# Kernel optimization log

Hardware: AMD Instinct MI355X
Metric: run time of the kernel (lower is better)

Reference implementation:

```python
import jax, jax.numpy as jnp
import numpy as np

N_NODES = 50000
N_EDGES = 800000
IN_F, HID_F, OUT_F = 96, 96, 32


def setup_inputs() -> dict:
    key = jax.random.key(0)
    k1, k2, k3, k4, k5 = jax.random.split(key, 5)
    x = jax.random.normal(k1, (N_NODES, IN_F), dtype=jnp.float32)
    src = jax.random.randint(k2, (N_EDGES,), 0, N_NODES, dtype=jnp.int32)
    dst = jax.random.randint(k3, (N_EDGES,), 0, N_NODES, dtype=jnp.int32)
    W1 = jax.random.normal(k4, (IN_F, HID_F), dtype=jnp.float32) / np.sqrt(IN_F)
    b1 = jnp.zeros((HID_F,), dtype=jnp.float32)
    W2 = jax.random.normal(k5, (HID_F, OUT_F), dtype=jnp.float32) / np.sqrt(HID_F)
    b2 = jnp.zeros((OUT_F,), dtype=jnp.float32)
    return {"x": x, "src": src, "dst": dst, "W1": W1, "b1": b1, "W2": W2, "b2": b2}


def _graph_conv(src, dst, n_nodes, h, W, b):
    # DGL GraphConv, norm='both': D_out^{-1/2} A D_in^{-1/2} h W + b
    ones = jnp.ones((src.shape[0],), dtype=h.dtype)
    deg_out = jax.ops.segment_sum(ones, src, num_segments=n_nodes)  # src out-degree
    deg_in = jax.ops.segment_sum(ones, dst, num_segments=n_nodes)   # dst in-degree
    norm_src = jax.lax.rsqrt(jnp.maximum(deg_out, 1.0))
    norm_dst = jax.lax.rsqrt(jnp.maximum(deg_in, 1.0))
    h = h * norm_src[:, None]
    msg = h[src]                                                    # [E, F] gather
    agg = jax.ops.segment_sum(msg, dst, num_segments=n_nodes)       # [N, F] scatter-add
    agg = agg * norm_dst[:, None]
    return agg @ W + b


def reference(x, src, dst, W1, b1, W2, b2):
    n = x.shape[0]
    h = _graph_conv(src, dst, n, x, W1, b1)
    h = jax.nn.relu(h)
    h = _graph_conv(src, dst, n, h, W2, b2)
    return h
```

## Files before the change

### kernel.cpp

```cpp
#include <hip/hip_runtime.h>


constexpr int NN = 50000;
constexpr int NE = 800000;
constexpr int CAP = 64;
constexpr int NNP = 50048;
constexpr int HN  = 25024;
constexpr int HW  = HN / 4;
constexpr int NCH = 2;
constexpr int NSL = 64;
constexpr int PREF_NB = (NN + 255) / 256;
constexpr int CVTW_NB = 48;
constexpr int FILL_NB = NCH * NSL;
constexpr int CVTX_NB = ((NN + 1) * 12 + 255) / 256;

using bf16x8 = __attribute__((ext_vector_type(8))) short;
using u16x8  = __attribute__((ext_vector_type(8))) unsigned short;
using f32x4  = __attribute__((ext_vector_type(4))) float;

__device__ __forceinline__ ushort f2b(float f) {
    unsigned u = __float_as_uint(f);
    u += 0x7FFFu + ((u >> 16) & 1u);
    return (ushort)(u >> 16);
}
__device__ __forceinline__ float b2f(ushort h) {
    return __uint_as_float(((unsigned)h) << 16);
}

__global__ void hist_kernel(const int* __restrict__ src, const int* __restrict__ dst,
                            unsigned char* __restrict__ pS, unsigned char* __restrict__ pD,
                            int ne) {
    __shared__ int binsS[HW];
    __shared__ int binsD[HW];
    const int ch = blockIdx.x, sl = blockIdx.y;
    const int lo = ch * HN;
    for (int i = threadIdx.x; i < HW; i += 256) { binsS[i] = 0; binsD[i] = 0; }
    __syncthreads();
    const int per4 = (ne / NSL) / 4;
    const int i0 = sl * per4;
    const int4* src4 = (const int4*)src;
    const int4* dst4 = (const int4*)dst;
    for (int i = i0 + threadIdx.x; i < i0 + per4; i += 256) {
        int4 s = src4[i];
        int4 d = dst4[i];
        unsigned u;
        u = (unsigned)(s.x - lo); if (u < HN) atomicAdd(binsS + (u >> 2), 1 << ((u & 3) * 8));
        u = (unsigned)(s.y - lo); if (u < HN) atomicAdd(binsS + (u >> 2), 1 << ((u & 3) * 8));
        u = (unsigned)(s.z - lo); if (u < HN) atomicAdd(binsS + (u >> 2), 1 << ((u & 3) * 8));
        u = (unsigned)(s.w - lo); if (u < HN) atomicAdd(binsS + (u >> 2), 1 << ((u & 3) * 8));
        u = (unsigned)(d.x - lo); if (u < HN) atomicAdd(binsD + (u >> 2), 1 << ((u & 3) * 8));
        u = (unsigned)(d.y - lo); if (u < HN) atomicAdd(binsD + (u >> 2), 1 << ((u & 3) * 8));
        u = (unsigned)(d.z - lo); if (u < HN) atomicAdd(binsD + (u >> 2), 1 << ((u & 3) * 8));
        u = (unsigned)(d.w - lo); if (u < HN) atomicAdd(binsD + (u >> 2), 1 << ((u & 3) * 8));
    }
    __syncthreads();
    int* oS = (int*)(pS + (size_t)sl * NNP + lo);
    int* oD = (int*)(pD + (size_t)sl * NNP + lo);
    for (int t = threadIdx.x; t < HW; t += 256) {
        oS[t] = binsS[t];
        oD[t] = binsD[t];
    }
}

__global__ void prefix_cvtw_kernel(const unsigned char* __restrict__ pS,
                                   unsigned char* __restrict__ pD,
                                   float* __restrict__ ns, int* __restrict__ cnt,
                                   const float* __restrict__ W1, const float* __restrict__ W2,
                                   ushort* __restrict__ W1t, ushort* __restrict__ W2t, int n) {
    int b = blockIdx.x;
    if (b < PREF_NB) {
        int i = b * 256 + threadIdx.x;
        if (i >= n) return;
        int sS = 0, run = 0;
#pragma unroll
        for (int sl = 0; sl < NSL; ++sl) {
            sS += pS[(size_t)sl * NNP + i];
            int c = pD[(size_t)sl * NNP + i];
            pD[(size_t)sl * NNP + i] = (unsigned char)run;
            run += c;
        }
        ns[i] = rsqrtf(fmaxf((float)sS, 1.0f));
        cnt[i] = run;
    } else {
        int i = (b - PREF_NB) * 256 + threadIdx.x;
        if (i < 96 * 96) {
            int k = i / 96, c = i % 96;
            W1t[c * 96 + k] = f2b(W1[i]);
        } else {
            int j = i - 96 * 96;
            int k = j / 32, c = j % 32;
            W2t[c * 96 + k] = f2b(W2[j]);
        }
    }
}

__global__ void fill_cvtx_kernel(const int* __restrict__ src, const int* __restrict__ dst,
                                 const unsigned char* __restrict__ pD,
                                 ushort* __restrict__ slots,
                                 const float* __restrict__ x, const float* __restrict__ ns,
                                 ushort* __restrict__ xh, int ne, int n) {
    __shared__ int cur[HW];
    int b = blockIdx.x;
    if (b < FILL_NB) {
        const int ch = b >> 6, sl = b & 63;
        const int lo = ch * HN;
        const int* ip = (const int*)(pD + (size_t)sl * NNP + lo);
        for (int t = threadIdx.x; t < HW; t += 256) cur[t] = ip[t];
        __syncthreads();
        const int per4 = (ne / NSL) / 4;
        const int i0 = sl * per4;
        const int4* src4 = (const int4*)src;
        const int4* dst4 = (const int4*)dst;
        for (int i = i0 + threadIdx.x; i < i0 + per4; i += 256) {
            int4 d = dst4[i];
            int4 s = src4[i];
            unsigned u; int sh, old, p;
            u = (unsigned)(d.x - lo);
            if (u < HN) { sh = (u & 3) * 8; old = atomicAdd(cur + (u >> 2), 1 << sh);
                p = (old >> sh) & 0xFF; if (p < CAP) slots[((size_t)(lo + u) << 6) + p] = (ushort)s.x; }
            u = (unsigned)(d.y - lo);
            if (u < HN) { sh = (u & 3) * 8; old = atomicAdd(cur + (u >> 2), 1 << sh);
                p = (old >> sh) & 0xFF; if (p < CAP) slots[((size_t)(lo + u) << 6) + p] = (ushort)s.y; }
            u = (unsigned)(d.z - lo);
            if (u < HN) { sh = (u & 3) * 8; old = atomicAdd(cur + (u >> 2), 1 << sh);
                p = (old >> sh) & 0xFF; if (p < CAP) slots[((size_t)(lo + u) << 6) + p] = (ushort)s.z; }
            u = (unsigned)(d.w - lo);
            if (u < HN) { sh = (u & 3) * 8; old = atomicAdd(cur + (u >> 2), 1 << sh);
                p = (old >> sh) & 0xFF; if (p < CAP) slots[((size_t)(lo + u) << 6) + p] = (ushort)s.w; }
        }
    } else {
        int t = (b - FILL_NB) * 256 + threadIdx.x;
        if (t >= (n + 1) * 12) return;
        int r = t / 12;
        u16x8 o;
        if (r == n) {
#pragma unroll
            for (int u = 0; u < 8; ++u) o[u] = 0;
        } else {
            float s = ns[r];
            const float4* p = (const float4*)(x) + (size_t)t * 2;
            float4 v0 = p[0], v1 = p[1];
            o[0] = f2b(s * v0.x); o[1] = f2b(s * v0.y); o[2] = f2b(s * v0.z); o[3] = f2b(s * v0.w);
            o[4] = f2b(s * v1.x); o[5] = f2b(s * v1.y); o[6] = f2b(s * v1.z); o[7] = f2b(s * v1.w);
        }
        *(u16x8*)&xh[(size_t)t * 8] = o;
    }
}

__global__ void agg1_kernel(const ushort* __restrict__ xh, const int* __restrict__ cnt,
                            const ushort* __restrict__ slots, ushort* __restrict__ AB, int n) {
    int tid = blockIdx.x * 256 + threadIdx.x;
    int r = tid / 12, q = tid % 12;
    if (r >= n) return;
    int deg = min(cnt[r], CAP);
    const ushort* br = slots + ((size_t)r << 6);
    float acc[8] = {};
    for (int j0 = 0; j0 < deg; j0 += 8) {
        u16x8 sl8 = *(const u16x8*)(br + j0);
        int s0 = (j0 + 0 < deg) ? (int)sl8[0] : n;
        int s1 = (j0 + 1 < deg) ? (int)sl8[1] : n;
        int s2 = (j0 + 2 < deg) ? (int)sl8[2] : n;
        int s3 = (j0 + 3 < deg) ? (int)sl8[3] : n;
        int s4 = (j0 + 4 < deg) ? (int)sl8[4] : n;
        int s5 = (j0 + 5 < deg) ? (int)sl8[5] : n;
        int s6 = (j0 + 6 < deg) ? (int)sl8[6] : n;
        int s7 = (j0 + 7 < deg) ? (int)sl8[7] : n;
        u16x8 v0 = *(const u16x8*)&xh[(size_t)s0 * 96 + q * 8];
        u16x8 v1 = *(const u16x8*)&xh[(size_t)s1 * 96 + q * 8];
        u16x8 v2 = *(const u16x8*)&xh[(size_t)s2 * 96 + q * 8];
        u16x8 v3 = *(const u16x8*)&xh[(size_t)s3 * 96 + q * 8];
        u16x8 v4 = *(const u16x8*)&xh[(size_t)s4 * 96 + q * 8];
        u16x8 v5 = *(const u16x8*)&xh[(size_t)s5 * 96 + q * 8];
        u16x8 v6 = *(const u16x8*)&xh[(size_t)s6 * 96 + q * 8];
        u16x8 v7 = *(const u16x8*)&xh[(size_t)s7 * 96 + q * 8];
#pragma unroll
        for (int t = 0; t < 8; ++t) acc[t] += b2f(v0[t]);
#pragma unroll
        for (int t = 0; t < 8; ++t) acc[t] += b2f(v1[t]);
#pragma unroll
        for (int t = 0; t < 8; ++t) acc[t] += b2f(v2[t]);
#pragma unroll
        for (int t = 0; t < 8; ++t) acc[t] += b2f(v3[t]);
#pragma unroll
        for (int t = 0; t < 8; ++t) acc[t] += b2f(v4[t]);
#pragma unroll
        for (int t = 0; t < 8; ++t) acc[t] += b2f(v5[t]);
#pragma unroll
        for (int t = 0; t < 8; ++t) acc[t] += b2f(v6[t]);
#pragma unroll
        for (int t = 0; t < 8; ++t) acc[t] += b2f(v7[t]);
    }
    u16x8 o;
#pragma unroll
    for (int t = 0; t < 8; ++t) o[t] = f2b(acc[t]);
    *(u16x8*)&AB[(size_t)r * 96 + q * 8] = o;
}

__global__ void __launch_bounds__(256) gemm12_fused(
        const ushort* __restrict__ AB, const ushort* __restrict__ W1t,
        const ushort* __restrict__ W2t, const float* __restrict__ b1,
        const float* __restrict__ ns, const int* __restrict__ cnt,
        ushort* __restrict__ t2h, int n) {
    __shared__ ushort Wl1[96 * 104];
    __shared__ ushort Wl2[32 * 104];
    __shared__ ushort Hl[64 * 104];
    for (int i = threadIdx.x; i < 1152; i += 256) {
        int nr = i / 12, k = (i % 12) * 8;
        *(bf16x8*)&Wl1[nr * 104 + k] = *(const bf16x8*)&W1t[nr * 96 + k];
    }
    for (int i = threadIdx.x; i < 384; i += 256) {
        int nr = i / 12, k = (i % 12) * 8;
        *(bf16x8*)&Wl2[nr * 104 + k] = *(const bf16x8*)&W2t[nr * 96 + k];
    }
    __syncthreads();

    const int lane = threadIdx.x & 63;
    const int w = threadIdx.x >> 6;
    const int rl = lane & 15, kg = lane >> 4;
    const int rowbase = blockIdx.x * 64 + w * 16;

    const ushort* arow = AB + (size_t)(rowbase + rl) * 96 + kg * 8;
    bf16x8 a0 = *(const bf16x8*)(arow);
    bf16x8 a1 = *(const bf16x8*)(arow + 32);
    bf16x8 a2 = *(const bf16x8*)(arow + 64);
    f32x4 acc1[6] = {};
#pragma unroll
    for (int nt = 0; nt < 6; ++nt) {
        const ushort* wr = &Wl1[(nt * 16 + rl) * 104 + kg * 8];
        acc1[nt] = __builtin_amdgcn_mfma_f32_16x16x32_bf16(a0, *(const bf16x8*)(wr),      acc1[nt], 0, 0, 0);
        acc1[nt] = __builtin_amdgcn_mfma_f32_16x16x32_bf16(a1, *(const bf16x8*)(wr + 32), acc1[nt], 0, 0, 0);
        acc1[nt] = __builtin_amdgcn_mfma_f32_16x16x32_bf16(a2, *(const bf16x8*)(wr + 64), acc1[nt], 0, 0, 0);
    }
    const int r0 = rowbase + kg * 4;
    float sj[4];
#pragma unroll
    for (int j = 0; j < 4; ++j) sj[j] = rsqrtf(fmaxf((float)cnt[r0 + j], 1.0f));
#pragma unroll
    for (int nt = 0; nt < 6; ++nt) {
        int col = nt * 16 + rl;
        float bc = b1[col];
#pragma unroll
        for (int j = 0; j < 4; ++j)
            Hl[(w * 16 + kg * 4 + j) * 104 + col] = f2b(fmaxf(acc1[nt][j] * sj[j] + bc, 0.f));
    }
    __syncthreads();

    const ushort* hrow = &Hl[(w * 16 + rl) * 104 + kg * 8];
    bf16x8 h0 = *(const bf16x8*)(hrow);
    bf16x8 h1 = *(const bf16x8*)(hrow + 32);
    bf16x8 h2 = *(const bf16x8*)(hrow + 64);
    f32x4 acc2[2] = {};
#pragma unroll
    for (int nt = 0; nt < 2; ++nt) {
        const ushort* wr = &Wl2[(nt * 16 + rl) * 104 + kg * 8];
        acc2[nt] = __builtin_amdgcn_mfma_f32_16x16x32_bf16(h0, *(const bf16x8*)(wr),      acc2[nt], 0, 0, 0);
        acc2[nt] = __builtin_amdgcn_mfma_f32_16x16x32_bf16(h1, *(const bf16x8*)(wr + 32), acc2[nt], 0, 0, 0);
        acc2[nt] = __builtin_amdgcn_mfma_f32_16x16x32_bf16(h2, *(const bf16x8*)(wr + 64), acc2[nt], 0, 0, 0);
    }
    float sn[4];
#pragma unroll
    for (int j = 0; j < 4; ++j) sn[j] = ns[r0 + j];
#pragma unroll
    for (int nt = 0; nt < 2; ++nt) {
        int col = nt * 16 + rl;
#pragma unroll
        for (int j = 0; j < 4; ++j) {
            float val = (r0 + j < n) ? acc2[nt][j] * sn[j] : 0.f;
            t2h[(size_t)(r0 + j) * 32 + col] = f2b(val);
        }
    }
}

__global__ void agg2_kernel(const ushort* __restrict__ t2h, const float* __restrict__ b2,
                            const int* __restrict__ cnt, const ushort* __restrict__ slots,
                            float* __restrict__ out, int n) {
    int tid = blockIdx.x * 256 + threadIdx.x;
    int r = tid / 4, q = tid % 4;
    if (r >= n) return;
    int deg = min(cnt[r], CAP);
    const ushort* br = slots + ((size_t)r << 6);
    float acc[8] = {};
    for (int j0 = 0; j0 < deg; j0 += 8) {
        u16x8 sl8 = *(const u16x8*)(br + j0);
        int s0 = (j0 + 0 < deg) ? (int)sl8[0] : n;
        int s1 = (j0 + 1 < deg) ? (int)sl8[1] : n;
        int s2 = (j0 + 2 < deg) ? (int)sl8[2] : n;
        int s3 = (j0 + 3 < deg) ? (int)sl8[3] : n;
        int s4 = (j0 + 4 < deg) ? (int)sl8[4] : n;
        int s5 = (j0 + 5 < deg) ? (int)sl8[5] : n;
        int s6 = (j0 + 6 < deg) ? (int)sl8[6] : n;
        int s7 = (j0 + 7 < deg) ? (int)sl8[7] : n;
        u16x8 v0 = *(const u16x8*)&t2h[(size_t)s0 * 32 + q * 8];
        u16x8 v1 = *(const u16x8*)&t2h[(size_t)s1 * 32 + q * 8];
        u16x8 v2 = *(const u16x8*)&t2h[(size_t)s2 * 32 + q * 8];
        u16x8 v3 = *(const u16x8*)&t2h[(size_t)s3 * 32 + q * 8];
        u16x8 v4 = *(const u16x8*)&t2h[(size_t)s4 * 32 + q * 8];
        u16x8 v5 = *(const u16x8*)&t2h[(size_t)s5 * 32 + q * 8];
        u16x8 v6 = *(const u16x8*)&t2h[(size_t)s6 * 32 + q * 8];
        u16x8 v7 = *(const u16x8*)&t2h[(size_t)s7 * 32 + q * 8];
#pragma unroll
        for (int t = 0; t < 8; ++t) acc[t] += b2f(v0[t]);
#pragma unroll
        for (int t = 0; t < 8; ++t) acc[t] += b2f(v1[t]);
#pragma unroll
        for (int t = 0; t < 8; ++t) acc[t] += b2f(v2[t]);
#pragma unroll
        for (int t = 0; t < 8; ++t) acc[t] += b2f(v3[t]);
#pragma unroll
        for (int t = 0; t < 8; ++t) acc[t] += b2f(v4[t]);
#pragma unroll
        for (int t = 0; t < 8; ++t) acc[t] += b2f(v5[t]);
#pragma unroll
        for (int t = 0; t < 8; ++t) acc[t] += b2f(v6[t]);
#pragma unroll
        for (int t = 0; t < 8; ++t) acc[t] += b2f(v7[t]);
    }
    float sd = rsqrtf(fmaxf((float)deg, 1.0f));
    const float4* bb = (const float4*)(b2 + q * 8);
    float4 bv0 = bb[0], bv1 = bb[1];
    float4 o0, o1;
    o0.x = acc[0] * sd + bv0.x; o0.y = acc[1] * sd + bv0.y;
    o0.z = acc[2] * sd + bv0.z; o0.w = acc[3] * sd + bv0.w;
    o1.x = acc[4] * sd + bv1.x; o1.y = acc[5] * sd + bv1.y;
    o1.z = acc[6] * sd + bv1.z; o1.w = acc[7] * sd + bv1.w;
    float4* po = (float4*)&out[(size_t)r * 32 + q * 8];
    po[0] = o0; po[1] = o1;
}

extern "C" void kernel_launch(void* const* d_in, const int* in_sizes, int n_in,
                              void* d_out, int out_size, void* d_ws, size_t ws_size,
                              hipStream_t stream) {
    const float* x   = (const float*)d_in[0];
    const int*   src = (const int*)d_in[1];
    const int*   dst = (const int*)d_in[2];
    const float* W1  = (const float*)d_in[3];
    const float* b1  = (const float*)d_in[4];
    const float* W2  = (const float*)d_in[5];
    const float* b2  = (const float*)d_in[6];
    float* out = (float*)d_out;

    int*    cnt   = (int*)d_ws;
    float*  ns    = (float*)(cnt + NNP);
    ushort* slots = (ushort*)(ns + NNP);
    unsigned char* pS = (unsigned char*)(slots + (size_t)NN * CAP);
    unsigned char* pD = pS + (size_t)NSL * NNP;
    ushort* xh    = (ushort*)(pD + (size_t)NSL * NNP);
    ushort* AB    = xh + (size_t)NNP * 96;
    ushort* t2h   = AB + (size_t)NNP * 96;
    ushort* W1t   = t2h + (size_t)NNP * 32;
    ushort* W2t   = W1t + 96 * 96;

    hist_kernel<<<dim3(NCH, NSL), 256, 0, stream>>>(src, dst, pS, pD, NE);
    prefix_cvtw_kernel<<<PREF_NB + CVTW_NB, 256, 0, stream>>>(pS, pD, ns, cnt, W1, W2, W1t, W2t, NN);
    fill_cvtx_kernel<<<FILL_NB + CVTX_NB, 256, 0, stream>>>(src, dst, pD, slots, x, ns, xh, NE, NN);

    agg1_kernel<<<(NN * 12 + 255) / 256, 256, 0, stream>>>(xh, cnt, slots, AB, NN);
    gemm12_fused<<<NNP / 64, 256, 0, stream>>>(AB, W1t, W2t, b1, ns, cnt, t2h, NN);
    agg2_kernel<<<(NN * 4 + 255) / 256, 256, 0, stream>>>(t2h, b2, cnt, slots, out, NN);
}
```

Baseline: 83.19 us.

## Fuse layer-1 aggregation into the GEMM kernel through shared memory

Merges the separate agg1 gather kernel into the fused GEMM kernel: each block aggregates its 64 rows of neighbour features into LDS, then runs both MFMA GEMMs from there. This removes the AB intermediate buffer's global write and read plus one kernel launch. It also drops the LDS staging of W1/W2 in favour of direct global (cache-resident) loads, and halves the gather unroll to 4 neighbours. Each block's 256 threads now handle 768 (row, slice) tasks in a loop, with less memory-level parallelism per thread and global weight loads inside the MFMA loop.

```diff
diff --git a/kernel.cpp b/kernel.cpp
--- a/kernel.cpp
+++ b/kernel.cpp
@@ -147,91 +147,64 @@
     }
 }
 
-__global__ void agg1_kernel(const ushort* __restrict__ xh, const int* __restrict__ cnt,
-                            const ushort* __restrict__ slots, ushort* __restrict__ AB, int n) {
-    int tid = blockIdx.x * 256 + threadIdx.x;
-    int r = tid / 12, q = tid % 12;
-    if (r >= n) return;
-    int deg = min(cnt[r], CAP);
-    const ushort* br = slots + ((size_t)r << 6);
-    float acc[8] = {};
-    for (int j0 = 0; j0 < deg; j0 += 8) {
-        u16x8 sl8 = *(const u16x8*)(br + j0);
-        int s0 = (j0 + 0 < deg) ? (int)sl8[0] : n;
-        int s1 = (j0 + 1 < deg) ? (int)sl8[1] : n;
-        int s2 = (j0 + 2 < deg) ? (int)sl8[2] : n;
-        int s3 = (j0 + 3 < deg) ? (int)sl8[3] : n;
-        int s4 = (j0 + 4 < deg) ? (int)sl8[4] : n;
-        int s5 = (j0 + 5 < deg) ? (int)sl8[5] : n;
-        int s6 = (j0 + 6 < deg) ? (int)sl8[6] : n;
-        int s7 = (j0 + 7 < deg) ? (int)sl8[7] : n;
-        u16x8 v0 = *(const u16x8*)&xh[(size_t)s0 * 96 + q * 8];
-        u16x8 v1 = *(const u16x8*)&xh[(size_t)s1 * 96 + q * 8];
-        u16x8 v2 = *(const u16x8*)&xh[(size_t)s2 * 96 + q * 8];
-        u16x8 v3 = *(const u16x8*)&xh[(size_t)s3 * 96 + q * 8];
-        u16x8 v4 = *(const u16x8*)&xh[(size_t)s4 * 96 + q * 8];
-        u16x8 v5 = *(const u16x8*)&xh[(size_t)s5 * 96 + q * 8];
-        u16x8 v6 = *(const u16x8*)&xh[(size_t)s6 * 96 + q * 8];
-        u16x8 v7 = *(const u16x8*)&xh[(size_t)s7 * 96 + q * 8];
-#pragma unroll
-        for (int t = 0; t < 8; ++t) acc[t] += b2f(v0[t]);
-#pragma unroll
-        for (int t = 0; t < 8; ++t) acc[t] += b2f(v1[t]);
-#pragma unroll
-        for (int t = 0; t < 8; ++t) acc[t] += b2f(v2[t]);
-#pragma unroll
-        for (int t = 0; t < 8; ++t) acc[t] += b2f(v3[t]);
-#pragma unroll
-        for (int t = 0; t < 8; ++t) acc[t] += b2f(v4[t]);
-#pragma unroll
-        for (int t = 0; t < 8; ++t) acc[t] += b2f(v5[t]);
-#pragma unroll
-        for (int t = 0; t < 8; ++t) acc[t] += b2f(v6[t]);
-#pragma unroll
-        for (int t = 0; t < 8; ++t) acc[t] += b2f(v7[t]);
-    }
-    u16x8 o;
-#pragma unroll
-    for (int t = 0; t < 8; ++t) o[t] = f2b(acc[t]);
-    *(u16x8*)&AB[(size_t)r * 96 + q * 8] = o;
-}
-
-__global__ void __launch_bounds__(256) gemm12_fused(
-        const ushort* __restrict__ AB, const ushort* __restrict__ W1t,
-        const ushort* __restrict__ W2t, const float* __restrict__ b1,
-        const float* __restrict__ ns, const int* __restrict__ cnt,
+__global__ void __launch_bounds__(256, 4) fused_aggemm(
+        const ushort* __restrict__ xh, const int* __restrict__ cnt,
+        const ushort* __restrict__ slots,
+        const ushort* __restrict__ W1t, const ushort* __restrict__ W2t,
+        const float* __restrict__ b1, const float* __restrict__ ns,
         ushort* __restrict__ t2h, int n) {
-    __shared__ ushort Wl1[96 * 104];
-    __shared__ ushort Wl2[32 * 104];
     __shared__ ushort Hl[64 * 104];
-    for (int i = threadIdx.x; i < 1152; i += 256) {
-        int nr = i / 12, k = (i % 12) * 8;
-        *(bf16x8*)&Wl1[nr * 104 + k] = *(const bf16x8*)&W1t[nr * 96 + k];
-    }
-    for (int i = threadIdx.x; i < 384; i += 256) {
-        int nr = i / 12, k = (i % 12) * 8;
-        *(bf16x8*)&Wl2[nr * 104 + k] = *(const bf16x8*)&W2t[nr * 96 + k];
+    const int rowbase0 = blockIdx.x * 64;
+
+    for (int u = threadIdx.x; u < 768; u += 256) {
+        int rl = u / 12, q = u % 12;
+        int r = rowbase0 + rl;
+        int deg = (r < n) ? min(cnt[r], CAP) : 0;
+        const ushort* br = slots + ((size_t)r << 6);
+        float acc[8] = {};
+        for (int j0 = 0; j0 < deg; j0 += 4) {
+            ushort4 sl4 = *(const ushort4*)(br + j0);
+            int s0 = (j0 + 0 < deg) ? (int)sl4.x : n;
+            int s1 = (j0 + 1 < deg) ? (int)sl4.y : n;
+            int s2 = (j0 + 2 < deg) ? (int)sl4.z : n;
+            int s3 = (j0 + 3 < deg) ? (int)sl4.w : n;
+            u16x8 v0 = *(const u16x8*)&xh[(size_t)s0 * 96 + q * 8];
+            u16x8 v1 = *(const u16x8*)&xh[(size_t)s1 * 96 + q * 8];
+            u16x8 v2 = *(const u16x8*)&xh[(size_t)s2 * 96 + q * 8];
+            u16x8 v3 = *(const u16x8*)&xh[(size_t)s3 * 96 + q * 8];
+#pragma unroll
+            for (int t = 0; t < 8; ++t) acc[t] += b2f(v0[t]);
+#pragma unroll
+            for (int t = 0; t < 8; ++t) acc[t] += b2f(v1[t]);
+#pragma unroll
+            for (int t = 0; t < 8; ++t) acc[t] += b2f(v2[t]);
+#pragma unroll
+            for (int t = 0; t < 8; ++t) acc[t] += b2f(v3[t]);
+        }
+        u16x8 o;
+#pragma unroll
+        for (int t = 0; t < 8; ++t) o[t] = f2b(acc[t]);
+        *(u16x8*)&Hl[rl * 104 + q * 8] = o;
     }
     __syncthreads();
 
     const int lane = threadIdx.x & 63;
     const int w = threadIdx.x >> 6;
     const int rl = lane & 15, kg = lane >> 4;
-    const int rowbase = blockIdx.x * 64 + w * 16;
-
-    const ushort* arow = AB + (size_t)(rowbase + rl) * 96 + kg * 8;
-    bf16x8 a0 = *(const bf16x8*)(arow);
-    bf16x8 a1 = *(const bf16x8*)(arow + 32);
-    bf16x8 a2 = *(const bf16x8*)(arow + 64);
+    const ushort* hrow = &Hl[(w * 16 + rl) * 104 + kg * 8];
+
+    bf16x8 a0 = *(const bf16x8*)(hrow);
+    bf16x8 a1 = *(const bf16x8*)(hrow + 32);
+    bf16x8 a2 = *(const bf16x8*)(hrow + 64);
     f32x4 acc1[6] = {};
 #pragma unroll
     for (int nt = 0; nt < 6; ++nt) {
-        const ushort* wr = &Wl1[(nt * 16 + rl) * 104 + kg * 8];
+        const ushort* wr = W1t + (nt * 16 + rl) * 96 + kg * 8;
         acc1[nt] = __builtin_amdgcn_mfma_f32_16x16x32_bf16(a0, *(const bf16x8*)(wr),      acc1[nt], 0, 0, 0);
         acc1[nt] = __builtin_amdgcn_mfma_f32_16x16x32_bf16(a1, *(const bf16x8*)(wr + 32), acc1[nt], 0, 0, 0);
         acc1[nt] = __builtin_amdgcn_mfma_f32_16x16x32_bf16(a2, *(const bf16x8*)(wr + 64), acc1[nt], 0, 0, 0);
     }
-    const int r0 = rowbase + kg * 4;
+    const int r0 = rowbase0 + w * 16 + kg * 4;
     float sj[4];
 #pragma unroll
     for (int j = 0; j < 4; ++j) sj[j] = rsqrtf(fmaxf((float)cnt[r0 + j], 1.0f));
@@ -245,14 +218,13 @@
     }
     __syncthreads();
 
-    const ushort* hrow = &Hl[(w * 16 + rl) * 104 + kg * 8];
     bf16x8 h0 = *(const bf16x8*)(hrow);
     bf16x8 h1 = *(const bf16x8*)(hrow + 32);
     bf16x8 h2 = *(const bf16x8*)(hrow + 64);
     f32x4 acc2[2] = {};
 #pragma unroll
     for (int nt = 0; nt < 2; ++nt) {
-        const ushort* wr = &Wl2[(nt * 16 + rl) * 104 + kg * 8];
+        const ushort* wr = W2t + (nt * 16 + rl) * 96 + kg * 8;
         acc2[nt] = __builtin_amdgcn_mfma_f32_16x16x32_bf16(h0, *(const bf16x8*)(wr),      acc2[nt], 0, 0, 0);
         acc2[nt] = __builtin_amdgcn_mfma_f32_16x16x32_bf16(h1, *(const bf16x8*)(wr + 32), acc2[nt], 0, 0, 0);
         acc2[nt] = __builtin_amdgcn_mfma_f32_16x16x32_bf16(h2, *(const bf16x8*)(wr + 64), acc2[nt], 0, 0, 0);
@@ -275,7 +247,7 @@
                             const int* __restrict__ cnt, const ushort* __restrict__ slots,
                             float* __restrict__ out, int n) {
     int tid = blockIdx.x * 256 + threadIdx.x;
-    int r = tid / 4, q = tid % 4;
+    int r = tid / 4, q = tid & 3;
     if (r >= n) return;
     int deg = min(cnt[r], CAP);
     const ushort* br = slots + ((size_t)r << 6);
@@ -345,8 +317,7 @@
     unsigned char* pS = (unsigned char*)(slots + (size_t)NN * CAP);
     unsigned char* pD = pS + (size_t)NSL * NNP;
     ushort* xh    = (ushort*)(pD + (size_t)NSL * NNP);
-    ushort* AB    = xh + (size_t)NNP * 96;
-    ushort* t2h   = AB + (size_t)NNP * 96;
+    ushort* t2h   = xh + (size_t)NNP * 96;
     ushort* W1t   = t2h + (size_t)NNP * 32;
     ushort* W2t   = W1t + 96 * 96;
 
@@ -354,7 +325,6 @@
     prefix_cvtw_kernel<<<PREF_NB + CVTW_NB, 256, 0, stream>>>(pS, pD, ns, cnt, W1, W2, W1t, W2t, NN);
     fill_cvtx_kernel<<<FILL_NB + CVTX_NB, 256, 0, stream>>>(src, dst, pD, slots, x, ns, xh, NE, NN);
 
-    agg1_kernel<<<(NN * 12 + 255) / 256, 256, 0, stream>>>(xh, cnt, slots, AB, NN);
-    gemm12_fused<<<NNP / 64, 256, 0, stream>>>(AB, W1t, W2t, b1, ns, cnt, t2h, NN);
+    fused_aggemm<<<NNP / 64, 256, 0, stream>>>(xh, cnt, slots, W1t, W2t, b1, ns, t2h, NN);
     agg2_kernel<<<(NN * 4 + 255) / 256, 256, 0, stream>>>(t2h, b2, cnt, slots, out, NN);
 }
```

After: 83.44 us. No clear change (+0.3%).
